# Kernel optimization log

Hardware: AMD Instinct MI355X
Metric: run time of the kernel (lower is better)

The kernel has to match this reference:

```python
import jax, jax.numpy as jnp
import numpy as np

N = 50000          # total_nodes (B*N diagonal-stacked graphs)
E = 800000         # total edges (avg degree 16)
HID = 128          # hidden_size
HEADS = 8          # num_heads


def setup_inputs() -> dict:
    key = jax.random.key(0)
    ks = jax.random.split(key, 10)
    s = 1.0 / np.sqrt(HID)
    x = jax.random.normal(ks[0], (N, HID), jnp.float32)
    edge_index = jax.random.randint(ks[1], (2, E), 0, N, dtype=jnp.int32).astype(jnp.int64)
    Wq = jax.random.normal(ks[2], (HID, HID), jnp.float32) * s
    bq = jax.random.normal(ks[3], (HID,), jnp.float32) * 0.01
    Wk = jax.random.normal(ks[4], (HID, HID), jnp.float32) * s
    bk = jax.random.normal(ks[5], (HID,), jnp.float32) * 0.01
    Wv = jax.random.normal(ks[6], (HID, HID), jnp.float32) * s
    bv = jax.random.normal(ks[7], (HID,), jnp.float32) * 0.01
    Wo = jax.random.normal(ks[8], (HID, HID), jnp.float32) * s
    bo = jax.random.normal(ks[9], (HID,), jnp.float32) * 0.01
    return {"x": x, "edge_index": edge_index, "total_nodes": N,
            "Wq": Wq, "bq": bq, "Wk": Wk, "bk": bk,
            "Wv": Wv, "bv": bv, "Wo": Wo, "bo": bo}


def reference(x, edge_index, total_nodes, Wq, bq, Wk, bk, Wv, bv, Wo, bo):
    H = HEADS
    D = HID // HEADS
    scale = D ** (-0.5)
    # torch Linear: y = x @ W.T + b
    Q = (x @ Wq.T + bq).reshape(-1, H, D)   # (N, H, D)
    K = (x @ Wk.T + bk).reshape(-1, H, D)
    V = (x @ Wv.T + bv).reshape(-1, H, D)
    src = edge_index[0]
    dst = edge_index[1]
    # edge-wise dot-product scores: (E, H)
    scores = jnp.einsum('ehd,ehd->eh', Q[dst], K[src]) * scale
    # scatter-softmax over edges sharing the same dst node
    mx = jax.ops.segment_max(scores, dst, num_segments=total_nodes)      # (N, H)
    ex = jnp.exp(scores - mx[dst])                                        # (E, H)
    se = jax.ops.segment_sum(ex, dst, num_segments=total_nodes)          # (N, H)
    attn = ex / (se[dst] + 1e-12)                                         # (E, H)
    # weighted message aggregation
    msg = attn[..., None] * V[src]                                        # (E, H, D)
    out = jax.ops.segment_sum(msg, dst, num_segments=total_nodes)        # (N, H, D)
    out = out.reshape(total_nodes, HID)
    return out @ Wo.T + bo
```

## Files before the change

### kernel.cpp

```cpp
#include <hip/hip_runtime.h>
#include <math.h>

#define NNODES 50000
#define NEDGES 800000
#define HIDDEN 128
#define NH 8
#define HD 16
#define CAP 64
#define NPART 8
#define PART_SZ 6250
#define SCAT_BPP 128
#define SCAT_BLOCKS (NPART * SCAT_BPP)
#define QKV_WAVES 6250
#define QKV_BLOCKS 1563

typedef __bf16 bf16x8 __attribute__((ext_vector_type(8)));
typedef float  f32x4  __attribute__((ext_vector_type(4)));

__device__ inline unsigned short f2b(float f) {
    unsigned u = __float_as_uint(f);
    unsigned r = (u + 0x7fffu + ((u >> 16) & 1u)) >> 16;
    return (unsigned short)r;
}

__device__ inline bf16x8 ld_a8(const float* __restrict__ p) {
    float4 a = *(const float4*)p;
    float4 b = *(const float4*)(p + 4);
    bf16x8 r;
    r[0] = (__bf16)a.x; r[1] = (__bf16)a.y; r[2] = (__bf16)a.z; r[3] = (__bf16)a.w;
    r[4] = (__bf16)b.x; r[5] = (__bf16)b.y; r[6] = (__bf16)b.z; r[7] = (__bf16)b.w;
    return r;
}

__global__ __launch_bounds__(256)
void pack_init(const float* __restrict__ Wq, const float* __restrict__ Wk,
               const float* __restrict__ Wv, const float* __restrict__ Wo,
               unsigned short* __restrict__ Pqkv, unsigned short* __restrict__ Po,
               int* __restrict__ cnt)
{
    if (blockIdx.x >= 32) {
        const int idx = (blockIdx.x - 32) * 256 + threadIdx.x;
        if (idx < NNODES / 4) ((int4*)cnt)[idx] = make_int4(0, 0, 0, 0);
        return;
    }
    const int s = blockIdx.x * 4 + (threadIdx.x >> 6);
    const int lane = threadIdx.x & 63;
    const float* W; unsigned short* P; int ct, c;
    if (s < 96) { ct = s >> 2; c = s & 3;
        W = (ct < 8) ? Wq : (ct < 16) ? Wk : Wv;
        P = Pqkv + (size_t)s * 512;
        ct &= 7;
    } else { int t = s - 96; ct = t >> 2; c = t & 3; W = Wo; P = Po + (size_t)t * 512; }
    const int colin = ct * 16 + (lane & 15);
    const int k0 = c * 32 + (lane >> 4) * 8;
    const float* sp = W + (size_t)colin * 128 + k0;
    unsigned short v[8];
#pragma unroll
    for (int j = 0; j < 8; ++j) v[j] = f2b(sp[j]);
    uint4 o;
    o.x = (unsigned)v[0] | ((unsigned)v[1] << 16);
    o.y = (unsigned)v[2] | ((unsigned)v[3] << 16);
    o.z = (unsigned)v[4] | ((unsigned)v[5] << 16);
    o.w = (unsigned)v[6] | ((unsigned)v[7] << 16);
    *(uint4*)(P + lane * 8) = o;
}

__global__ __launch_bounds__(256)
void qkv_scatter(const float* __restrict__ x, const unsigned short* __restrict__ Pqkv,
                 const float* __restrict__ bq, const float* __restrict__ bk,
                 const float* __restrict__ bv,
                 const int* __restrict__ src, const int* __restrict__ dst,
                 unsigned short* __restrict__ Qb, unsigned short* __restrict__ KVb,
                 int* __restrict__ cnt, int* __restrict__ bucket)
{
    if (blockIdx.x >= QKV_BLOCKS) {
        const int sb = blockIdx.x - QKV_BLOCKS;
        const int part = sb & (NPART - 1);
        const int blk  = sb >> 3;
        const int lo = part * PART_SZ, hi = lo + PART_SZ;
        for (int e = blk * 256 + threadIdx.x; e < NEDGES; e += SCAT_BPP * 256) {
            const int d = dst[e];
            if (d >= lo && d < hi) {
                const int pos = atomicAdd(&cnt[d], 1);
                if (pos < CAP) bucket[d * CAP + pos] = src[e];
            }
        }
        return;
    }

    const int w = blockIdx.x * 4 + (threadIdx.x >> 6);
    if (w >= QKV_WAVES) return;
    const int lane = threadIdx.x & 63;
    const int band = w >> 1, half = w & 1;
    const int row0 = band * 16;
    const int ar = lane & 15, kg = lane >> 4;

    const float* ap = x + (size_t)(row0 + ar) * 128 + kg * 8;
    const bf16x8 a0 = ld_a8(ap);
    const bf16x8 a1 = ld_a8(ap + 32);
    const bf16x8 a2 = ld_a8(ap + 64);
    const bf16x8 a3 = ld_a8(ap + 96);

    const unsigned short* wp = Pqkv + (size_t)(half * 48) * 512 + lane * 8;
    bf16x8 nb0 = *(const bf16x8*)(wp);
    bf16x8 nb1 = *(const bf16x8*)(wp + 512);
    bf16x8 nb2 = *(const bf16x8*)(wp + 1024);
    bf16x8 nb3 = *(const bf16x8*)(wp + 1536);

#pragma unroll
    for (int t = 0; t < 12; ++t) {
        const bf16x8 b0 = nb0, b1 = nb1, b2 = nb2, b3 = nb3;
        if (t < 11) {
            const unsigned short* nw = wp + (size_t)(t + 1) * 2048;
            nb0 = *(const bf16x8*)(nw);
            nb1 = *(const bf16x8*)(nw + 512);
            nb2 = *(const bf16x8*)(nw + 1024);
            nb3 = *(const bf16x8*)(nw + 1536);
        }
        f32x4 acc = {0.f, 0.f, 0.f, 0.f};
        acc = __builtin_amdgcn_mfma_f32_16x16x32_bf16(a0, b0, acc, 0, 0, 0);
        acc = __builtin_amdgcn_mfma_f32_16x16x32_bf16(a1, b1, acc, 0, 0, 0);
        acc = __builtin_amdgcn_mfma_f32_16x16x32_bf16(a2, b2, acc, 0, 0, 0);
        acc = __builtin_amdgcn_mfma_f32_16x16x32_bf16(a3, b3, acc, 0, 0, 0);

        const int ct = half * 12 + t;
        const int sel = ct >> 3;
        const int colin = (ct & 7) * 16 + ar;
        if (sel == 0) {
            const float bsc = bq[colin];
#pragma unroll
            for (int j = 0; j < 4; ++j)
                Qb[(size_t)(row0 + kg * 4 + j) * 128 + colin] = f2b(acc[j] + bsc);
        } else {
            const float bsc = (sel == 1) ? bk[colin] : bv[colin];
            const int koff = (sel == 2) ? 2 : 0;
            const int cbase = (colin >> 1) * 4 + (colin & 1) + koff;
#pragma unroll
            for (int j = 0; j < 4; ++j)
                KVb[(size_t)(row0 + kg * 4 + j) * 256 + cbase] = f2b(acc[j] + bsc);
        }
    }
}

__global__ __launch_bounds__(256)
void fused_attn_kernel(const unsigned short* __restrict__ Qb,
                       const unsigned short* __restrict__ KVb,
                       const int* __restrict__ cnt, const int* __restrict__ bucket,
                       unsigned short* __restrict__ accumb)
{
    const int wave = threadIdx.x >> 6;
    const int lane = threadIdx.x & 63;
    const int n = blockIdx.x * 4 + wave;
    if (n >= NNODES) return;

    int deg = cnt[n];
    deg = deg > CAP ? CAP : deg;
    const int mysrc = (lane < deg) ? bucket[n * CAP + lane] : 0;

    const unsigned short* kvbase = KVb + lane * 4;

    const unsigned qw = *(const unsigned*)(Qb + (size_t)n * HIDDEN + lane * 2);
    const float qx = __uint_as_float(qw << 16) * 0.25f;
    const float qy = __uint_as_float(qw & 0xffff0000u) * 0.25f;

    float m = -INFINITY, s = 0.f, ox = 0.f, oy = 0.f;

    uint2 kvA = make_uint2(0,0), kvB = kvA, kvC = kvA, kvD = kvA;
    if (deg > 0) kvA = *(const uint2*)(kvbase + ((size_t)__shfl(mysrc, 0) << 8));
    if (deg > 1) kvB = *(const uint2*)(kvbase + ((size_t)__shfl(mysrc, 1) << 8));
    if (deg > 2) kvC = *(const uint2*)(kvbase + ((size_t)__shfl(mysrc, 2) << 8));
    if (deg > 3) kvD = *(const uint2*)(kvbase + ((size_t)__shfl(mysrc, 3) << 8));

    int i = 0;
    for (; i + 2 <= deg; i += 2) {
        const uint2 c0 = kvA, c1 = kvB;
        kvA = kvC; kvB = kvD;
        if (i + 4 < deg) kvC = *(const uint2*)(kvbase + ((size_t)__shfl(mysrc, i + 4) << 8));
        if (i + 5 < deg) kvD = *(const uint2*)(kvbase + ((size_t)__shfl(mysrc, i + 5) << 8));

        float d0 = qx * __uint_as_float(c0.x << 16) + qy * __uint_as_float(c0.x & 0xffff0000u);
        float d1 = qx * __uint_as_float(c1.x << 16) + qy * __uint_as_float(c1.x & 0xffff0000u);
        d0 += __shfl_xor(d0, 1);  d1 += __shfl_xor(d1, 1);
        d0 += __shfl_xor(d0, 2);  d1 += __shfl_xor(d1, 2);
        d0 += __shfl_xor(d0, 4);  d1 += __shfl_xor(d1, 4);

        const float pm = fmaxf(d0, d1);
        const float ee = __expf(-fabsf(d0 - d1));
        const bool g = d0 >= d1;
        const float v0x = __uint_as_float(c0.y << 16), v0y = __uint_as_float(c0.y & 0xffff0000u);
        const float v1x = __uint_as_float(c1.y << 16), v1y = __uint_as_float(c1.y & 0xffff0000u);
        const float sp  = 1.f + ee;
        const float ovx = fmaf(ee, g ? v1x : v0x, g ? v0x : v1x);
        const float ovy = fmaf(ee, g ? v1y : v0y, g ? v0y : v1y);

        const float dd = pm - m;
        const float em = __expf(-fabsf(dd));
        const bool nm = dd > 0.f;
        const float so = nm ? em : 1.f;
        const float sn = nm ? 1.f : em;
        m = nm ? pm : m;
        s  = fmaf(s,  so, sp  * sn);
        ox = fmaf(ox, so, ovx * sn);
        oy = fmaf(oy, so, ovy * sn);
    }
    if (i < deg) {
        const uint2 c0 = kvA;
        float d0 = qx * __uint_as_float(c0.x << 16) + qy * __uint_as_float(c0.x & 0xffff0000u);
        d0 += __shfl_xor(d0, 1);
        d0 += __shfl_xor(d0, 2);
        d0 += __shfl_xor(d0, 4);
        const float vx = __uint_as_float(c0.y << 16), vy = __uint_as_float(c0.y & 0xffff0000u);
        const float dd = d0 - m;
        const float em = __expf(-fabsf(dd));
        const bool nm = dd > 0.f;
        const float so = nm ? em : 1.f;
        const float pp = nm ? 1.f : em;
        m = nm ? d0 : m;
        s  = fmaf(s,  so, pp);
        ox = fmaf(ox, so, pp * vx);
        oy = fmaf(oy, so, pp * vy);
    }
    const float inv = 1.f / (s + 1e-12f);
    ushort2 ob = { f2b(ox * inv), f2b(oy * inv) };
    *(ushort2*)(accumb + (size_t)n * HIDDEN + lane * 2) = ob;
}

__global__ __launch_bounds__(256)
void outproj_mfma(const unsigned short* __restrict__ accumb, const unsigned short* __restrict__ Po,
                  const float* __restrict__ bo, float* __restrict__ out)
{
    const int band = blockIdx.x * 4 + (threadIdx.x >> 6);
    if (band >= 3125) return;
    const int lane = threadIdx.x & 63;
    const int row0 = band * 16;
    const int ar = lane & 15, kg = lane >> 4;

    const unsigned short* ab = accumb + (size_t)(row0 + ar) * 128 + kg * 8;
    const bf16x8 a0 = *(const bf16x8*)(ab);
    const bf16x8 a1 = *(const bf16x8*)(ab + 32);
    const bf16x8 a2 = *(const bf16x8*)(ab + 64);
    const bf16x8 a3 = *(const bf16x8*)(ab + 96);

    const unsigned short* wp = Po + lane * 8;
    bf16x8 nb0 = *(const bf16x8*)(wp);
    bf16x8 nb1 = *(const bf16x8*)(wp + 512);
    bf16x8 nb2 = *(const bf16x8*)(wp + 1024);
    bf16x8 nb3 = *(const bf16x8*)(wp + 1536);

#pragma unroll
    for (int t = 0; t < 8; ++t) {
        const bf16x8 b0 = nb0, b1 = nb1, b2 = nb2, b3 = nb3;
        if (t < 7) {
            const unsigned short* nw = wp + (size_t)(t + 1) * 2048;
            nb0 = *(const bf16x8*)(nw);
            nb1 = *(const bf16x8*)(nw + 512);
            nb2 = *(const bf16x8*)(nw + 1024);
            nb3 = *(const bf16x8*)(nw + 1536);
        }
        f32x4 acc = {0.f, 0.f, 0.f, 0.f};
        acc = __builtin_amdgcn_mfma_f32_16x16x32_bf16(a0, b0, acc, 0, 0, 0);
        acc = __builtin_amdgcn_mfma_f32_16x16x32_bf16(a1, b1, acc, 0, 0, 0);
        acc = __builtin_amdgcn_mfma_f32_16x16x32_bf16(a2, b2, acc, 0, 0, 0);
        acc = __builtin_amdgcn_mfma_f32_16x16x32_bf16(a3, b3, acc, 0, 0, 0);

        const int colin = t * 16 + ar;
        const float bsc = bo[colin];
#pragma unroll
        for (int j = 0; j < 4; ++j)
            out[(size_t)(row0 + kg * 4 + j) * 128 + colin] = acc[j] + bsc;
    }
}

extern "C" void kernel_launch(void* const* d_in, const int* in_sizes, int n_in,
                              void* d_out, int out_size, void* d_ws, size_t ws_size,
                              hipStream_t stream) {
    const float* x  = (const float*)d_in[0];
    const int*   ei = (const int*)d_in[1];
    const int*   src = ei;
    const int*   dst = ei + NEDGES;
    const float* Wq = (const float*)d_in[3];
    const float* bq = (const float*)d_in[4];
    const float* Wk = (const float*)d_in[5];
    const float* bk = (const float*)d_in[6];
    const float* Wv = (const float*)d_in[7];
    const float* bv = (const float*)d_in[8];
    const float* Wo = (const float*)d_in[9];
    const float* bo = (const float*)d_in[10];
    float* out = (float*)d_out;

    char* ws = (char*)d_ws;
    size_t off = 0;
    const size_t sz_nhb = (size_t)NNODES * HIDDEN * sizeof(unsigned short);
    unsigned short* Qb     = (unsigned short*)(ws + off); off += sz_nhb;
    unsigned short* KVb    = (unsigned short*)(ws + off); off += 2 * sz_nhb;
    unsigned short* accumb = (unsigned short*)(ws + off); off += sz_nhb;
    unsigned short* Pqkv   = (unsigned short*)(ws + off); off += 96 * 512 * sizeof(unsigned short);
    unsigned short* Po     = (unsigned short*)(ws + off); off += 32 * 512 * sizeof(unsigned short);
    int*            cnt    = (int*)(ws + off);            off += (size_t)NNODES * sizeof(int);
    int*            bucket = (int*)(ws + off);            off += (size_t)NNODES * CAP * sizeof(int);

    pack_init<<<81, 256, 0, stream>>>(Wq, Wk, Wv, Wo, Pqkv, Po, cnt);

    qkv_scatter<<<QKV_BLOCKS + SCAT_BLOCKS, 256, 0, stream>>>(
        x, Pqkv, bq, bk, bv, src, dst, Qb, KVb, cnt, bucket);

    fused_attn_kernel<<<(NNODES + 3) / 4, 256, 0, stream>>>(Qb, KVb, cnt, bucket, accumb);

    outproj_mfma<<<782, 256, 0, stream>>>(accumb, Po, bo, out);
}
```

Baseline: 139.2 us.

## Remap attention lanes to head×edge-slot with full-head K/V vector loads

```diff
diff --git a/kernel.cpp b/kernel.cpp
--- a/kernel.cpp
+++ b/kernel.cpp
@@ -11,8 +11,7 @@
 #define PART_SZ 6250
 #define SCAT_BPP 128
 #define SCAT_BLOCKS (NPART * SCAT_BPP)
-#define QKV_WAVES 6250
-#define QKV_BLOCKS 1563
+#define QKV_BLOCKS 782
 
 typedef __bf16 bf16x8 __attribute__((ext_vector_type(8)));
 typedef float  f32x4  __attribute__((ext_vector_type(4)));
@@ -30,6 +29,13 @@
     r[0] = (__bf16)a.x; r[1] = (__bf16)a.y; r[2] = (__bf16)a.z; r[3] = (__bf16)a.w;
     r[4] = (__bf16)b.x; r[5] = (__bf16)b.y; r[6] = (__bf16)b.z; r[7] = (__bf16)b.w;
     return r;
+}
+
+__device__ inline void up8(const uint4 u, float* f) {
+    f[0] = __uint_as_float(u.x << 16); f[1] = __uint_as_float(u.x & 0xffff0000u);
+    f[2] = __uint_as_float(u.y << 16); f[3] = __uint_as_float(u.y & 0xffff0000u);
+    f[4] = __uint_as_float(u.z << 16); f[5] = __uint_as_float(u.z & 0xffff0000u);
+    f[6] = __uint_as_float(u.w << 16); f[7] = __uint_as_float(u.w & 0xffff0000u);
 }
 
 __global__ __launch_bounds__(256)
@@ -89,10 +95,9 @@
     }
 
     const int w = blockIdx.x * 4 + (threadIdx.x >> 6);
-    if (w >= QKV_WAVES) return;
+    if (w >= 3125) return;
     const int lane = threadIdx.x & 63;
-    const int band = w >> 1, half = w & 1;
-    const int row0 = band * 16;
+    const int row0 = w * 16;
     const int ar = lane & 15, kg = lane >> 4;
 
     const float* ap = x + (size_t)(row0 + ar) * 128 + kg * 8;
@@ -101,16 +106,16 @@
     const bf16x8 a2 = ld_a8(ap + 64);
     const bf16x8 a3 = ld_a8(ap + 96);
 
-    const unsigned short* wp = Pqkv + (size_t)(half * 48) * 512 + lane * 8;
+    const unsigned short* wp = Pqkv + lane * 8;
     bf16x8 nb0 = *(const bf16x8*)(wp);
     bf16x8 nb1 = *(const bf16x8*)(wp + 512);
     bf16x8 nb2 = *(const bf16x8*)(wp + 1024);
     bf16x8 nb3 = *(const bf16x8*)(wp + 1536);
 
 #pragma unroll
-    for (int t = 0; t < 12; ++t) {
+    for (int t = 0; t < 24; ++t) {
         const bf16x8 b0 = nb0, b1 = nb1, b2 = nb2, b3 = nb3;
-        if (t < 11) {
+        if (t < 23) {
             const unsigned short* nw = wp + (size_t)(t + 1) * 2048;
             nb0 = *(const bf16x8*)(nw);
             nb1 = *(const bf16x8*)(nw + 512);
@@ -123,21 +128,23 @@
         acc = __builtin_amdgcn_mfma_f32_16x16x32_bf16(a2, b2, acc, 0, 0, 0);
         acc = __builtin_amdgcn_mfma_f32_16x16x32_bf16(a3, b3, acc, 0, 0, 0);
 
-        const int ct = half * 12 + t;
-        const int sel = ct >> 3;
-        const int colin = (ct & 7) * 16 + ar;
+        const int sel = t >> 3;
+        const int colin = (t & 7) * 16 + ar;
         if (sel == 0) {
             const float bsc = bq[colin];
 #pragma unroll
             for (int j = 0; j < 4; ++j)
                 Qb[(size_t)(row0 + kg * 4 + j) * 128 + colin] = f2b(acc[j] + bsc);
+        } else if (sel == 1) {
+            const float bsc = bk[colin];
+#pragma unroll
+            for (int j = 0; j < 4; ++j)
+                KVb[(size_t)(row0 + kg * 4 + j) * 256 + colin] = f2b(acc[j] + bsc);
         } else {
-            const float bsc = (sel == 1) ? bk[colin] : bv[colin];
-            const int koff = (sel == 2) ? 2 : 0;
-            const int cbase = (colin >> 1) * 4 + (colin & 1) + koff;
+            const float bsc = bv[colin];
 #pragma unroll
             for (int j = 0; j < 4; ++j)
-                KVb[(size_t)(row0 + kg * 4 + j) * 256 + cbase] = f2b(acc[j] + bsc);
+                KVb[(size_t)(row0 + kg * 4 + j) * 256 + 128 + colin] = f2b(acc[j] + bsc);
         }
     }
 }
@@ -153,76 +160,107 @@
     const int n = blockIdx.x * 4 + wave;
     if (n >= NNODES) return;
 
-    int deg = cnt[n];
-    deg = deg > CAP ? CAP : deg;
+    const int h = lane >> 3;
+    const int slot = lane & 7;
+
+    int deg = cnt[n]; deg = deg > CAP ? CAP : deg;
     const int mysrc = (lane < deg) ? bucket[n * CAP + lane] : 0;
 
-    const unsigned short* kvbase = KVb + lane * 4;
-
-    const unsigned qw = *(const unsigned*)(Qb + (size_t)n * HIDDEN + lane * 2);
-    const float qx = __uint_as_float(qw << 16) * 0.25f;
-    const float qy = __uint_as_float(qw & 0xffff0000u) * 0.25f;
-
-    float m = -INFINITY, s = 0.f, ox = 0.f, oy = 0.f;
-
-    uint2 kvA = make_uint2(0,0), kvB = kvA, kvC = kvA, kvD = kvA;
-    if (deg > 0) kvA = *(const uint2*)(kvbase + ((size_t)__shfl(mysrc, 0) << 8));
-    if (deg > 1) kvB = *(const uint2*)(kvbase + ((size_t)__shfl(mysrc, 1) << 8));
-    if (deg > 2) kvC = *(const uint2*)(kvbase + ((size_t)__shfl(mysrc, 2) << 8));
-    if (deg > 3) kvD = *(const uint2*)(kvbase + ((size_t)__shfl(mysrc, 3) << 8));
-
-    int i = 0;
-    for (; i + 2 <= deg; i += 2) {
-        const uint2 c0 = kvA, c1 = kvB;
-        kvA = kvC; kvB = kvD;
-        if (i + 4 < deg) kvC = *(const uint2*)(kvbase + ((size_t)__shfl(mysrc, i + 4) << 8));
-        if (i + 5 < deg) kvD = *(const uint2*)(kvbase + ((size_t)__shfl(mysrc, i + 5) << 8));
-
-        float d0 = qx * __uint_as_float(c0.x << 16) + qy * __uint_as_float(c0.x & 0xffff0000u);
-        float d1 = qx * __uint_as_float(c1.x << 16) + qy * __uint_as_float(c1.x & 0xffff0000u);
-        d0 += __shfl_xor(d0, 1);  d1 += __shfl_xor(d1, 1);
-        d0 += __shfl_xor(d0, 2);  d1 += __shfl_xor(d1, 2);
-        d0 += __shfl_xor(d0, 4);  d1 += __shfl_xor(d1, 4);
-
-        const float pm = fmaxf(d0, d1);
-        const float ee = __expf(-fabsf(d0 - d1));
-        const bool g = d0 >= d1;
-        const float v0x = __uint_as_float(c0.y << 16), v0y = __uint_as_float(c0.y & 0xffff0000u);
-        const float v1x = __uint_as_float(c1.y << 16), v1y = __uint_as_float(c1.y & 0xffff0000u);
-        const float sp  = 1.f + ee;
-        const float ovx = fmaf(ee, g ? v1x : v0x, g ? v0x : v1x);
-        const float ovy = fmaf(ee, g ? v1y : v0y, g ? v0y : v1y);
-
-        const float dd = pm - m;
-        const float em = __expf(-fabsf(dd));
-        const bool nm = dd > 0.f;
-        const float so = nm ? em : 1.f;
-        const float sn = nm ? 1.f : em;
-        m = nm ? pm : m;
-        s  = fmaf(s,  so, sp  * sn);
-        ox = fmaf(ox, so, ovx * sn);
-        oy = fmaf(oy, so, ovy * sn);
-    }
-    if (i < deg) {
-        const uint2 c0 = kvA;
-        float d0 = qx * __uint_as_float(c0.x << 16) + qy * __uint_as_float(c0.x & 0xffff0000u);
-        d0 += __shfl_xor(d0, 1);
-        d0 += __shfl_xor(d0, 2);
-        d0 += __shfl_xor(d0, 4);
-        const float vx = __uint_as_float(c0.y << 16), vy = __uint_as_float(c0.y & 0xffff0000u);
-        const float dd = d0 - m;
+    float q[16];
+    {
+        const uint4* qp = (const uint4*)(Qb + (size_t)n * HIDDEN + h * 16);
+        up8(qp[0], q); up8(qp[1], q + 8);
+#pragma unroll
+        for (int j = 0; j < 16; ++j) q[j] *= 0.25f;
+    }
+
+    float m = -1e30f, s = 0.f;
+    float o[16];
+#pragma unroll
+    for (int j = 0; j < 16; ++j) o[j] = 0.f;
+
+    const int nit = (deg + 7) >> 3;
+    const uint4 zz = make_uint4(0, 0, 0, 0);
+    uint4 k0 = zz, k1 = zz, v0 = zz, v1 = zz;
+    if (slot < deg) {
+        const int sid = __shfl(mysrc, slot);
+        const uint4* kp = (const uint4*)(KVb + (size_t)sid * 256 + h * 16);
+        k0 = kp[0]; k1 = kp[1];
+        const uint4* vp = (const uint4*)(KVb + (size_t)sid * 256 + 128 + h * 16);
+        v0 = vp[0]; v1 = vp[1];
+    }
+
+    for (int i = 0; i < nit; ++i) {
+        uint4 nk0 = zz, nk1 = zz, nv0 = zz, nv1 = zz;
+        const int nidx = i * 8 + 8 + slot;
+        if (nidx < deg) {
+            const int sid = __shfl(mysrc, nidx);
+            const uint4* kp = (const uint4*)(KVb + (size_t)sid * 256 + h * 16);
+            nk0 = kp[0]; nk1 = kp[1];
+            const uint4* vp = (const uint4*)(KVb + (size_t)sid * 256 + 128 + h * 16);
+            nv0 = vp[0]; nv1 = vp[1];
+        }
+        float kk[16], vv[16];
+        up8(k0, kk); up8(k1, kk + 8);
+        up8(v0, vv); up8(v1, vv + 8);
+
+        float d0 = 0.f, d1 = 0.f, d2 = 0.f, d3 = 0.f;
+#pragma unroll
+        for (int j = 0; j < 16; j += 4) {
+            d0 = fmaf(q[j],     kk[j],     d0);
+            d1 = fmaf(q[j + 1], kk[j + 1], d1);
+            d2 = fmaf(q[j + 2], kk[j + 2], d2);
+            d3 = fmaf(q[j + 3], kk[j + 3], d3);
+        }
+        float score = (d0 + d1) + (d2 + d3);
+        if (i * 8 + slot >= deg) score = -2e30f;
+
+        const float dd = score - m;
         const float em = __expf(-fabsf(dd));
         const bool nm = dd > 0.f;
         const float so = nm ? em : 1.f;
         const float pp = nm ? 1.f : em;
-        m = nm ? d0 : m;
-        s  = fmaf(s,  so, pp);
-        ox = fmaf(ox, so, pp * vx);
-        oy = fmaf(oy, so, pp * vy);
-    }
-    const float inv = 1.f / (s + 1e-12f);
-    ushort2 ob = { f2b(ox * inv), f2b(oy * inv) };
-    *(ushort2*)(accumb + (size_t)n * HIDDEN + lane * 2) = ob;
+        m = nm ? score : m;
+        s = fmaf(s, so, pp);
+#pragma unroll
+        for (int j = 0; j < 16; ++j)
+            o[j] = fmaf(o[j], so, pp * vv[j]);
+
+        k0 = nk0; k1 = nk1; v0 = nv0; v1 = nv1;
+    }
+
+#pragma unroll
+    for (int mask = 1; mask <= 4; mask <<= 1) {
+        const float om = __shfl_xor(m, mask);
+        const float dd = om - m;
+        const float em = __expf(-fabsf(dd));
+        const bool nm = dd > 0.f;
+        const float so = nm ? em : 1.f;
+        const float oo = nm ? 1.f : em;
+        m = nm ? om : m;
+        const float os = __shfl_xor(s, mask);
+        s = fmaf(s, so, os * oo);
+#pragma unroll
+        for (int j = 0; j < 16; ++j) {
+            const float oj = __shfl_xor(o[j], mask);
+            o[j] = fmaf(o[j], so, oj * oo);
+        }
+    }
+
+    if (slot == 0) {
+        const float inv = 1.f / (s + 1e-12f);
+        uint4 w0, w1;
+        w0.x = (unsigned)f2b(o[0]  * inv) | ((unsigned)f2b(o[1]  * inv) << 16);
+        w0.y = (unsigned)f2b(o[2]  * inv) | ((unsigned)f2b(o[3]  * inv) << 16);
+        w0.z = (unsigned)f2b(o[4]  * inv) | ((unsigned)f2b(o[5]  * inv) << 16);
+        w0.w = (unsigned)f2b(o[6]  * inv) | ((unsigned)f2b(o[7]  * inv) << 16);
+        w1.x = (unsigned)f2b(o[8]  * inv) | ((unsigned)f2b(o[9]  * inv) << 16);
+        w1.y = (unsigned)f2b(o[10] * inv) | ((unsigned)f2b(o[11] * inv) << 16);
+        w1.z = (unsigned)f2b(o[12] * inv) | ((unsigned)f2b(o[13] * inv) << 16);
+        w1.w = (unsigned)f2b(o[14] * inv) | ((unsigned)f2b(o[15] * inv) << 16);
+        uint4* op = (uint4*)(accumb + (size_t)n * HIDDEN + h * 16);
+        op[0] = w0; op[1] = w1;
+    }
 }
 
 __global__ __launch_bounds__(256)
```

Result: no change. 137.6 us (-1.1%).
